# Kernel tuning notes

Measured on AMD Instinct MI355X. Metric: run time of the kernel, lower is better.

## Reference

```python
import jax, jax.numpy as jnp
import numpy as np

HEAD = 32  # HEAD_SIZE
B, T, C = 8, 1024, 768
LAYER_ID, N_LAYER = 2, 12


def wkv7(r, w, k, v, a, b):
    # RWKV7 linear recurrence (matches the custom CUDA 'attn' kernel math):
    #   S = S * exp(-exp(w)) + (S @ a) b^T + v k^T ;  y = S @ r
    Bb, Tt, Cc = r.shape
    H, N = Cc // HEAD, HEAD
    rs = lambda z: jnp.moveaxis(z.reshape(Bb, Tt, H, N), 1, 0)  # [T,B,H,N]
    rT, kT, vT, aT, bT = rs(r), rs(k), rs(v), rs(a), rs(b)
    wT = rs(jnp.exp(-jnp.exp(w)))  # decay in (0,1)
    def step(S, inp):
        rt, wt, kt, vt, at, bt = inp  # each [B,H,N]
        sa = jnp.einsum('bhij,bhj->bhi', S, at)
        S = S * wt[:, :, None, :] + sa[..., None] * bt[:, :, None, :] + vt[..., None] * kt[:, :, None, :]
        return S, jnp.einsum('bhij,bhj->bhi', S, rt)
    S0 = jnp.zeros((Bb, H, N, N), r.dtype)
    _, y = jax.lax.scan(step, S0, (rT, wT, kT, vT, aT, bT))
    return jnp.moveaxis(y, 0, 1).reshape(Bb, Tt, Cc)


def setup_inputs() -> dict:
    key = jax.random.key(0)
    ks = iter(jax.random.split(key, 64))
    def rn(shape, s=0.02):
        return (jax.random.normal(next(ks), shape, jnp.float32) * s)
    def un(shape, lim):
        return jax.random.uniform(next(ks), shape, jnp.float32, -lim, lim)
    H, N = C // HEAD, HEAD
    r10 = 1.0 - LAYER_ID / N_LAYER          # ratio_1_to_almost0
    r01 = LAYER_ID / (N_LAYER - 1)          # ratio_0_to_1
    ddd = (np.arange(C, dtype=np.float64) / C).reshape(1, 1, C)
    f32 = lambda z: jnp.asarray(z, jnp.float32)
    time_maa_x = f32(1.0 - ddd ** (0.6 * r10 ** 0.9))
    time_maa_rg = f32(1.0 - ddd ** (0.2 * r10))
    time_maa_wa = f32(1.0 - ddd ** (0.9 * r10))
    time_maa_k = f32(1.0 - (ddd ** (0.9 * r10) + 0.4 * r01))
    time_maa_v = f32(1.0 - (ddd ** (0.4 * r10) + 0.6 * r01))
    ds = -7.0 + 5.0 * (np.arange(C, dtype=np.float64) / (C - 1)) ** (0.85 + r01 ** 0.5)
    time_decay = f32(ds.reshape(1, 1, C) + 0.5)
    inp = {
        'x': jax.random.normal(next(ks), (B, T, C), jnp.float32),
        'v1': jax.random.normal(next(ks), (B, T, C), jnp.float32),
        'time_maa_x': time_maa_x, 'time_maa_rg': time_maa_rg, 'time_maa_wa': time_maa_wa,
        'time_maa_k': time_maa_k, 'time_maa_v': time_maa_v,
        'time_decay': time_decay,
        'time_faaaa': rn((1, 1, H, N), 0.05),
        'time_aaaaa': rn((1, 1, C), 0.05),
        'time_maa_w1': rn((C, 28 * 4)), 'time_maa_w2': rn((4, 28, C), 0.05),
        'time_decay_w1': rn((C, 64)), 'time_decay_w2': rn((64, C), 0.05),
        'time_aaa_w1': rn((C, 24)), 'time_aaa_w2': rn((24, C), 0.05),
        'time_kkk_w1': rn((C, 24)), 'time_kkk_w2': rn((24, C), 0.05),
        'gate_w1': rn((C, 120)), 'gate_w2': rn((120, C), 0.05),
        'ma_w1': rn((C, 24)), 'ma_w2': rn((24, C), 0.05), 'time_misc_a': rn((1, 1, C), 0.05),
        'mk_w1': rn((C, 24)), 'mk_w2': rn((24, C), 0.05), 'time_misc_k': rn((1, 1, C), 0.05),
        'mv_w1': rn((C, 24)), 'mv_w2': rn((24, C), 0.05), 'time_misc_v': 1.0 + rn((1, 1, C), 0.05),
        'Wr': un((C, C), 0.5 / C ** 0.5), 'Wk': un((C, C), 0.05 / C ** 0.5),
        'Wv': un((C, C), 0.5 / C ** 0.5), 'Wo': rn((C, C), 0.02),
        'ln_w': jnp.ones((C,), jnp.float32), 'ln_b': jnp.zeros((C,), jnp.float32),
    }
    return inp


def reference(x, v1, time_maa_x, time_maa_rg, time_maa_wa, time_maa_k, time_maa_v,
              time_decay, time_faaaa, time_aaaaa, time_maa_w1, time_maa_w2,
              time_decay_w1, time_decay_w2, time_aaa_w1, time_aaa_w2,
              time_kkk_w1, time_kkk_w2, gate_w1, gate_w2, ma_w1, ma_w2, time_misc_a,
              mk_w1, mk_w2, time_misc_k, mv_w1, mv_w2, time_misc_v,
              Wr, Wk, Wv, Wo, ln_w, ln_b):
    Bb, Tt, Cc = x.shape
    H, N = Cc // HEAD, HEAD
    # token shift: xx[t] = x[t-1] - x[t], with x[-1] = 0
    xsh = jnp.concatenate([jnp.zeros_like(x[:, :1]), x[:, :-1]], axis=1)
    xx = xsh - x
    xxx = x + xx * time_maa_x
    tm = jnp.tanh(xxx @ time_maa_w1).reshape(Bb, Tt, 4, -1)      # [B,T,4,28]
    mix = jnp.einsum('btfd,fdc->fbtc', tm, time_maa_w2)          # [4,B,T,C]
    xrg = x + xx * (time_maa_rg + mix[0])
    xwa = x + xx * (time_maa_wa + mix[1])
    xk = x + xx * (time_maa_k + mix[2])
    xv = x + xx * (time_maa_v + mix[3])
    r = xrg @ Wr
    w = -jax.nn.softplus(-(time_decay + jnp.tanh(xwa @ time_decay_w1) @ time_decay_w2)) - 0.5
    k = xk @ Wk
    v = xv @ Wv
    v = v + (v1 - v) * jax.nn.sigmoid(time_misc_v + xv @ mv_w1 @ mv_w2)
    g = jax.nn.sigmoid(xrg @ gate_w1) @ gate_w2
    kk = k + jnp.tanh(xk @ time_kkk_w1) @ time_kkk_w2
    kk4 = kk.reshape(Bb, Tt, H, N)
    nrm = jnp.maximum(jnp.sqrt(jnp.sum(kk4 * kk4, axis=-1, keepdims=True)), 1e-12)
    kk = (kk4 / nrm).reshape(Bb, Tt, Cc)
    a = jax.nn.sigmoid(time_aaaaa + xwa @ time_aaa_w1 @ time_aaa_w2)
    ma = jax.nn.sigmoid(time_misc_a + xwa @ ma_w1 @ ma_w2)
    k = k * ma + k * a * (1.0 - ma)
    mk = jax.nn.sigmoid(time_misc_k + xk @ mk_w1 @ mk_w2)
    k = k * jnp.exp(jnp.minimum(w * mk, 0.0))
    y = wkv7(r, w, k, v, -kk, kk * a)
    # GroupNorm(n_head groups) over each token, eps=6.4e-5
    yg = y.reshape(Bb, Tt, H, N)
    mu = jnp.mean(yg, axis=-1, keepdims=True)
    var = jnp.var(yg, axis=-1, keepdims=True)
    yn = (yg - mu) * jax.lax.rsqrt(var + 6.4e-05)
    yn = yn * ln_w.reshape(H, N) + ln_b.reshape(H, N)
    # per-head bonus term
    bonus = (jnp.sum(r.reshape(Bb, Tt, H, N) * k.reshape(Bb, Tt, H, N) * time_faaaa,
                     axis=-1, keepdims=True) * v.reshape(Bb, Tt, H, N))
    y = yn.reshape(Bb, Tt, Cc) + bonus.reshape(Bb, Tt, Cc)
    out = (y * g) @ Wo
    return (out, v1)
```

## Files before the change

### kernel.cpp

```cpp
#include <hip/hip_runtime.h>
#include <hip/hip_bf16.h>
#include <math.h>

#define Bdim 8
#define Tdim 1024
#define Cdim 768
#define Hdim 24
#define Ndim 32
#define BTdim (Bdim*Tdim)
#define CH6 16

typedef __attribute__((ext_vector_type(8))) short bf16x8;
typedef __attribute__((ext_vector_type(4))) float f32x4;
typedef __hip_bfloat16 bf16;

__device__ __forceinline__ float sigm(float x){ return 1.f/(1.f+expf(-x)); }
__device__ __forceinline__ float softplusf(float x){ return fmaxf(x,0.f) + log1pf(expf(-fabsf(x))); }
__device__ __forceinline__ float bf2f(bf16 v){ return __bfloat162float(v); }
__device__ __forceinline__ float us2f(unsigned short s){ return __builtin_bit_cast(float, (unsigned)s<<16); }

template<int CTRL>
__device__ __forceinline__ float dpp_add(float x){
  int xi = __builtin_bit_cast(int, x);
  int yi = __builtin_amdgcn_mov_dpp(xi, CTRL, 0xF, 0xF, true);
  return x + __builtin_bit_cast(float, yi);
}
__device__ __forceinline__ float red32(float x){
  x = dpp_add<0xB1>(x);
  x = dpp_add<0x4E>(x);
  x = dpp_add<0x141>(x);
  x = dpp_add<0x140>(x);
  x += __shfl_xor(x, 16);
  return x;
}
__device__ __forceinline__ float red16(float x){
  x = dpp_add<0xB1>(x);
  x = dpp_add<0x4E>(x);
  x = dpp_add<0x141>(x);
  x = dpp_add<0x140>(x);
  return x;
}
__device__ __forceinline__ void cvt8(uint4 u, float* d){
  d[0]=__builtin_bit_cast(float, u.x<<16); d[1]=__builtin_bit_cast(float, u.x&0xFFFF0000u);
  d[2]=__builtin_bit_cast(float, u.y<<16); d[3]=__builtin_bit_cast(float, u.y&0xFFFF0000u);
  d[4]=__builtin_bit_cast(float, u.z<<16); d[5]=__builtin_bit_cast(float, u.z&0xFFFF0000u);
  d[6]=__builtin_bit_cast(float, u.w<<16); d[7]=__builtin_bit_cast(float, u.w&0xFFFF0000u);
}

#define GLDS16(gp, lp) __builtin_amdgcn_global_load_lds((const __attribute__((address_space(1))) void*)(gp), (__attribute__((address_space(3))) void*)(lp), 16, 0, 0)

__global__ void k1_shift(const float* __restrict__ x, const float* __restrict__ maa_x,
                         float* __restrict__ xx, bf16* __restrict__ xxx) {
  int idx = blockIdx.x*256 + threadIdx.x;
  if (idx >= BTdim*Cdim) return;
  int c = idx % Cdim; int row = idx / Cdim; int t = row % Tdim;
  float xv = x[idx];
  float xp = (t==0) ? 0.f : x[idx - Cdim];
  float d = xp - xv;
  xx[idx] = d;
  xxx[idx] = __float2bfloat16(xv + d*maa_x[c]);
}

__global__ __launch_bounds__(256) void kconvW(const float* __restrict__ W0, const float* __restrict__ W1,
    const float* __restrict__ W2, const float* __restrict__ W3,
    bf16* __restrict__ T0, bf16* __restrict__ T1, bf16* __restrict__ T2, bf16* __restrict__ T3) {
  const float* Wsrc[4] = {W0,W1,W2,W3};
  bf16* Tdst[4] = {T0,T1,T2,T3};
  const float* W = Wsrc[blockIdx.z];
  bf16* T = Tdst[blockIdx.z];
  __shared__ float tile[32][33];
  int bx = blockIdx.x*32, by = blockIdx.y*32;
  int tx = threadIdx.x & 31, ty = threadIdx.x >> 5;
  #pragma unroll
  for (int q=0;q<32;q+=8) tile[ty+q][tx] = W[(size_t)(by+ty+q)*Cdim + bx+tx];
  __syncthreads();
  #pragma unroll
  for (int q=0;q<32;q+=8) T[(size_t)(bx+ty+q)*Cdim + by+tx] = __float2bfloat16(tile[tx][ty+q]);
}

__global__ __launch_bounds__(256) void kprep(const float* __restrict__ dw1, const float* __restrict__ aaa_w1,
    const float* __restrict__ ma_w1, const float* __restrict__ kkk_w1, const float* __restrict__ mk_w1,
    const float* __restrict__ mv_w1, const float* __restrict__ gate_w1, const float* __restrict__ maa_w1,
    const float* __restrict__ dw2, const float* __restrict__ aaa_w2, const float* __restrict__ ma_w2,
    const float* __restrict__ kkk_w2, const float* __restrict__ mk_w2, const float* __restrict__ mv_w2,
    const float* __restrict__ gate_w2,
    bf16* __restrict__ PWwa, bf16* __restrict__ PWk, bf16* __restrict__ PWv,
    bf16* __restrict__ PWrg, bf16* __restrict__ PWmaa,
    bf16* __restrict__ W2wa, bf16* __restrict__ W2k, bf16* __restrict__ W2v, bf16* __restrict__ W2g){
  int idx = blockIdx.x*256 + threadIdx.x;
  if (idx < 491520) {
    int buf = idx / 98304, rem = idx - buf*98304;
    int n = rem / 768, kk = rem - n*768;
    float val = 0.f;
    bf16* dst;
    switch(buf){
      case 0: dst=PWwa; if(n<64) val=dw1[(size_t)kk*64+n]; else if(n<88) val=aaa_w1[(size_t)kk*24+(n-64)]; else if(n<112) val=ma_w1[(size_t)kk*24+(n-88)]; break;
      case 1: dst=PWk;  if(n<24) val=kkk_w1[(size_t)kk*24+n]; else if(n<48) val=mk_w1[(size_t)kk*24+(n-24)]; break;
      case 2: dst=PWv;  if(n<24) val=mv_w1[(size_t)kk*24+n]; break;
      case 3: dst=PWrg; if(n<120) val=gate_w1[(size_t)kk*120+n]; break;
      default: dst=PWmaa; if(n<112) val=maa_w1[(size_t)kk*112+n]; break;
    }
    dst[rem] = __float2bfloat16(val);
    return;
  }
  int i = idx - 491520;
  if (i < 294912){
    int n=i>>7, q=i&127, seg=n/768, c=n-seg*768;
    float val=0.f;
    if (seg==0){ if(q<64) val=dw2[(size_t)q*768+c]; }
    else if (seg==1){ if(q>=64&&q<88) val=aaa_w2[(size_t)(q-64)*768+c]; }
    else { if(q>=88&&q<112) val=ma_w2[(size_t)(q-88)*768+c]; }
    W2wa[i]=__float2bfloat16(val); return;
  }
  i -= 294912;
  if (i < 98304){
    int n=i>>6, q=i&63, seg=n/768, c=n-seg*768;
    float val=0.f;
    if (seg==0){ if(q<24) val=kkk_w2[(size_t)q*768+c]; }
    else { if(q>=24&&q<48) val=mk_w2[(size_t)(q-24)*768+c]; }
    W2k[i]=__float2bfloat16(val); return;
  }
  i -= 98304;
  if (i < 24576){
    int c=i>>5, q=i&31;
    float val = (q<24) ? mv_w2[(size_t)q*768+c] : 0.f;
    W2v[i]=__float2bfloat16(val); return;
  }
  i -= 24576;
  if (i < 98304){
    int c=i>>7, q=i&127;
    float val = (q<120) ? gate_w2[(size_t)q*768+c] : 0.f;
    W2g[i]=__float2bfloat16(val);
  }
}

template<typename OutT>
__global__ __launch_bounds__(256) void gemm_mfma(const bf16* __restrict__ A,
    const bf16* __restrict__ Bt, OutT* __restrict__ C, int M, int N, int K) {
  __shared__ unsigned short As[128*32];
  __shared__ unsigned short Bs[128*32];
  const int bm = blockIdx.y*128, bn = blockIdx.x*128;
  const int tid = threadIdx.x, lane = tid&63, w = tid>>6;
  const int wr = w>>1, wc = w&1;
  const int lr = lane&15, kg = lane>>4;
  f32x4 zero = {0.f,0.f,0.f,0.f};
  f32x4 acc[4][4];
  #pragma unroll
  for (int m=0;m<4;m++)
    #pragma unroll
    for (int n=0;n<4;n++) acc[m][n]=zero;
  const size_t rowA = (size_t)(bm + w*32 + (lane>>2))*K + (lane&3)*8;
  const size_t rowB = (size_t)(bn + w*32 + (lane>>2))*K + (lane&3)*8;
  unsigned short* lA = As + w*32*32;
  unsigned short* lB = Bs + w*32*32;
  for (int k0=0; k0<K; k0+=32){
    GLDS16(A + rowA + k0,                 lA);
    GLDS16(A + rowA + k0 + (size_t)16*K,  lA + 512);
    GLDS16(Bt + rowB + k0,                lB);
    GLDS16(Bt + rowB + k0 + (size_t)16*K, lB + 512);
    __syncthreads();
    bf16x8 af[4], bfr[4];
    #pragma unroll
    for (int m=0;m<4;m++) af[m]  = *(const bf16x8*)(void*)(As + (wr*64+m*16+lr)*32 + kg*8);
    #pragma unroll
    for (int n=0;n<4;n++) bfr[n] = *(const bf16x8*)(void*)(Bs + (wc*64+n*16+lr)*32 + kg*8);
    #pragma unroll
    for (int m=0;m<4;m++)
      #pragma unroll
      for (int n=0;n<4;n++)
        acc[m][n] = __builtin_amdgcn_mfma_f32_16x16x32_bf16(af[m], bfr[n], acc[m][n], 0,0,0);
    __syncthreads();
  }
  #pragma unroll
  for (int m=0;m<4;m++)
    #pragma unroll
    for (int n=0;n<4;n++){
      size_t r0 = (size_t)(bm + wr*64 + m*16 + kg*4);
      int cc = bn + wc*64 + n*16 + lr;
      #pragma unroll
      for (int q=0;q<4;q++){
        float val = acc[m][n][q];
        if constexpr (sizeof(OutT)==2) C[(r0+q)*N + cc] = __float2bfloat16(val);
        else                           C[(r0+q)*N + cc] = val;
      }
    }
}

__global__ __launch_bounds__(256) void gemm_tm(const bf16* __restrict__ A,
    const bf16* __restrict__ Bt, float* __restrict__ C, int K) {
  __shared__ unsigned short As[128*32];
  __shared__ unsigned short Bs[128*32];
  const int bm = blockIdx.y*128;
  const int tid = threadIdx.x, lane = tid&63, w = tid>>6;
  const int wr = w>>1, wc = w&1;
  const int lr = lane&15, kg = lane>>4;
  f32x4 zero = {0.f,0.f,0.f,0.f};
  f32x4 acc[4][4];
  #pragma unroll
  for (int m=0;m<4;m++)
    #pragma unroll
    for (int n=0;n<4;n++) acc[m][n]=zero;
  const size_t rowA = (size_t)(bm + w*32 + (lane>>2))*K + (lane&3)*8;
  const size_t rowB = (size_t)(w*32 + (lane>>2))*K + (lane&3)*8;
  unsigned short* lA = As + w*32*32;
  unsigned short* lB = Bs + w*32*32;
  for (int k0=0; k0<K; k0+=32){
    GLDS16(A + rowA + k0,                 lA);
    GLDS16(A + rowA + k0 + (size_t)16*K,  lA + 512);
    GLDS16(Bt + rowB + k0,                lB);
    GLDS16(Bt + rowB + k0 + (size_t)16*K, lB + 512);
    __syncthreads();
    bf16x8 af[4], bfr[4];
    #pragma unroll
    for (int m=0;m<4;m++) af[m]  = *(const bf16x8*)(void*)(As + (wr*64+m*16+lr)*32 + kg*8);
    #pragma unroll
    for (int n=0;n<4;n++) bfr[n] = *(const bf16x8*)(void*)(Bs + (wc*64+n*16+lr)*32 + kg*8);
    #pragma unroll
    for (int m=0;m<4;m++)
      #pragma unroll
      for (int n=0;n<4;n++)
        acc[m][n] = __builtin_amdgcn_mfma_f32_16x16x32_bf16(af[m], bfr[n], acc[m][n], 0,0,0);
    __syncthreads();
  }
  #pragma unroll
  for (int m=0;m<4;m++)
    #pragma unroll
    for (int n=0;n<4;n++){
      size_t r0 = (size_t)(bm + wr*64 + m*16 + kg*4);
      int cc = wc*64 + n*16 + lr;
      if (cc < 112){
        #pragma unroll
        for (int q=0;q<4;q++)
          C[(r0+q)*112 + cc] = tanhf(acc[m][n][q]);
      }
    }
}

struct S1P {
  const bf16* A[4];
  const bf16* Bt[4];
  bf16* C[4];
  int Ntrue[4];
  int Nalloc[4];
  int act[4];
};
__global__ __launch_bounds__(256) void gemm_s1(S1P p, int K) {
  const int z = blockIdx.z;
  const bf16* __restrict__ A  = p.A[z];
  const bf16* __restrict__ Bt = p.Bt[z];
  bf16* __restrict__ C = p.C[z];
  const int Ntrue = p.Ntrue[z], Nalloc = p.Nalloc[z], act = p.act[z];
  __shared__ unsigned short As[128*32];
  __shared__ unsigned short Bs[128*32];
  const int bm = blockIdx.y*128;
  const int tid = threadIdx.x, lane = tid&63, w = tid>>6;
  const int wr = w>>1, wc = w&1;
  const int lr = lane&15, kg = lane>>4;
  f32x4 zero = {0.f,0.f,0.f,0.f};
  f32x4 acc[4][4];
  #pragma unroll
  for (int m=0;m<4;m++)
    #pragma unroll
    for (int n=0;n<4;n++) acc[m][n]=zero;
  const size_t rowA = (size_t)(bm + w*32 + (lane>>2))*K + (lane&3)*8;
  const size_t rowB = (size_t)(w*32 + (lane>>2))*K + (lane&3)*8;
  unsigned short* lA = As + w*32*32;
  unsigned short* lB = Bs + w*32*32;
  for (int k0=0; k0<K; k0+=32){
    GLDS16(A + rowA + k0,                 lA);
    GLDS16(A + rowA + k0 + (size_t)16*K,  lA + 512);
    GLDS16(Bt + rowB + k0,                lB);
    GLDS16(Bt + rowB + k0 + (size_t)16*K, lB + 512);
    __syncthreads();
    bf16x8 af[4], bfr[4];
    #pragma unroll
    for (int m=0;m<4;m++) af[m]  = *(const bf16x8*)(void*)(As + (wr*64+m*16+lr)*32 + kg*8);
    #pragma unroll
    for (int n=0;n<4;n++) bfr[n] = *(const bf16x8*)(void*)(Bs + (wc*64+n*16+lr)*32 + kg*8);
    #pragma unroll
    for (int m=0;m<4;m++)
      #pragma unroll
      for (int n=0;n<4;n++)
        acc[m][n] = __builtin_amdgcn_mfma_f32_16x16x32_bf16(af[m], bfr[n], acc[m][n], 0,0,0);
    __syncthreads();
  }
  #pragma unroll
  for (int m=0;m<4;m++)
    #pragma unroll
    for (int n=0;n<4;n++){
      size_t r0 = (size_t)(bm + wr*64 + m*16 + kg*4);
      int cc = wc*64 + n*16 + lr;
      if (cc < Nalloc){
        #pragma unroll
        for (int q=0;q<4;q++){
          float val = acc[m][n][q];
          if      (act==1){ if (cc<64) val = tanhf(val); }
          else if (act==2){ if (cc<24) val = tanhf(val); }
          else if (act==3){ val = sigm(val); }
          if (cc >= Ntrue) val = 0.f;
          C[(r0+q)*Nalloc + cc] = __float2bfloat16(val);
        }
      }
    }
}

struct Z4 {
  const bf16* A[4];
  const bf16* Bt[4];
  bf16* C[4];
  int N[4];
  int K[4];
};
__global__ __launch_bounds__(256) void gemm_z(Z4 p) {
  const int z = blockIdx.z;
  const int N = p.N[z], K = p.K[z];
  const int bn = blockIdx.x*128;
  if (bn >= N) return;
  const bf16* __restrict__ A  = p.A[z];
  const bf16* __restrict__ Bt = p.Bt[z];
  bf16* __restrict__ C = p.C[z];
  __shared__ unsigned short As[128*32];
  __shared__ unsigned short Bs[128*32];
  const int bm = blockIdx.y*128;
  const int tid = threadIdx.x, lane = tid&63, w = tid>>6;
  const int wr = w>>1, wc = w&1;
  const int lr = lane&15, kg = lane>>4;
  f32x4 zero = {0.f,0.f,0.f,0.f};
  f32x4 acc[4][4];
  #pragma unroll
  for (int m=0;m<4;m++)
    #pragma unroll
    for (int n=0;n<4;n++) acc[m][n]=zero;
  const size_t rowA = (size_t)(bm + w*32 + (lane>>2))*K + (lane&3)*8;
  const size_t rowB = (size_t)(bn + w*32 + (lane>>2))*K + (lane&3)*8;
  unsigned short* lA = As + w*32*32;
  unsigned short* lB = Bs + w*32*32;
  for (int k0=0; k0<K; k0+=32){
    GLDS16(A + rowA + k0,                 lA);
    GLDS16(A + rowA + k0 + (size_t)16*K,  lA + 512);
    GLDS16(Bt + rowB + k0,                lB);
    GLDS16(Bt + rowB + k0 + (size_t)16*K, lB + 512);
    __syncthreads();
    bf16x8 af[4], bfr[4];
    #pragma unroll
    for (int m=0;m<4;m++) af[m]  = *(const bf16x8*)(void*)(As + (wr*64+m*16+lr)*32 + kg*8);
    #pragma unroll
    for (int n=0;n<4;n++) bfr[n] = *(const bf16x8*)(void*)(Bs + (wc*64+n*16+lr)*32 + kg*8);
    #pragma unroll
    for (int m=0;m<4;m++)
      #pragma unroll
      for (int n=0;n<4;n++)
        acc[m][n] = __builtin_amdgcn_mfma_f32_16x16x32_bf16(af[m], bfr[n], acc[m][n], 0,0,0);
    __syncthreads();
  }
  #pragma unroll
  for (int m=0;m<4;m++)
    #pragma unroll
    for (int n=0;n<4;n++){
      size_t r0 = (size_t)(bm + wr*64 + m*16 + kg*4);
      int cc = bn + wc*64 + n*16 + lr;
      #pragma unroll
      for (int q=0;q<4;q++)
        C[(r0+q)*N + cc] = __float2bfloat16(acc[m][n][q]);
    }
}

__global__ __launch_bounds__(256) void k2_mix(const float* __restrict__ x, const float* __restrict__ xx,
    const float* __restrict__ tm, const float* __restrict__ w2,
    const float* __restrict__ mrg, const float* __restrict__ mwa,
    const float* __restrict__ mk_, const float* __restrict__ mv_,
    bf16* __restrict__ xrg, bf16* __restrict__ xwa, bf16* __restrict__ xk, bf16* __restrict__ xv) {
  const int row0 = blockIdx.x*8, tid = threadIdx.x;
  __shared__ float stm[8][112];
  for (int idx=tid; idx<8*112; idx+=256){
    int rr=idx/112, q=idx-rr*112;
    stm[rr][q]=tm[(size_t)(row0+rr)*112+q];
  }
  __syncthreads();
  for (int c=tid;c<Cdim;c+=256){
    float x8[8], d8[8];
    #pragma unroll
    for (int rr=0;rr<8;rr++){
      size_t i=(size_t)(row0+rr)*Cdim+c;
      x8[rr]=x[i]; d8[rr]=xx[i];
    }
    float mrgc=mrg[c], mwac=mwa[c], mkc=mk_[c], mvc=mv_[c];
    float m0[8]={},m1[8]={},m2[8]={},m3[8]={};
    #pragma unroll 4
    for (int d=0; d<28; d++){
      float w0=w2[(size_t)(d)*Cdim + c];
      float w1=w2[(size_t)(28+d)*Cdim + c];
      float w2v=w2[(size_t)(56+d)*Cdim + c];
      float w3=w2[(size_t)(84+d)*Cdim + c];
      #pragma unroll
      for (int rr=0;rr<8;rr++){
        m0[rr]+=stm[rr][d]*w0; m1[rr]+=stm[rr][28+d]*w1;
        m2[rr]+=stm[rr][56+d]*w2v; m3[rr]+=stm[rr][84+d]*w3;
      }
    }
    #pragma unroll
    for (int rr=0;rr<8;rr++){
      size_t i=(size_t)(row0+rr)*Cdim+c;
      xrg[i]=__float2bfloat16(x8[rr] + d8[rr]*(mrgc+m0[rr]));
      xwa[i]=__float2bfloat16(x8[rr] + d8[rr]*(mwac+m1[rr]));
      xk[i] =__float2bfloat16(x8[rr] + d8[rr]*(mkc+m2[rr]));
      xv[i] =__float2bfloat16(x8[rr] + d8[rr]*(mvc+m3[rr]));
    }
  }
}

__global__ __launch_bounds__(256) void k5_fuse(
    const bf16* __restrict__ zwa, const bf16* __restrict__ zk, const bf16* __restrict__ zv,
    const float* __restrict__ td, const float* __restrict__ aaaaa,
    const float* __restrict__ misc_a, const float* __restrict__ misc_k, const float* __restrict__ misc_v,
    const float* __restrict__ v1,
    float* __restrict__ kbuf, float* __restrict__ vbuf, float* __restrict__ wexp,
    bf16* __restrict__ kb_bf, bf16* __restrict__ vb_bf,
    bf16* __restrict__ akv, bf16* __restrict__ bkv) {
  const int row = blockIdx.x, tid = threadIdx.x;
  float kraw[3], v0[3], v1v[3];
  #pragma unroll
  for (int it=0;it<3;it++){
    size_t i=(size_t)row*Cdim + tid + it*256;
    kraw[it]=kbuf[i]; v0[it]=vbuf[i]; v1v[it]=v1[i];
  }
  __syncthreads();
  #pragma unroll
  for (int it=0;it<3;it++){
    const int c = tid + it*256;
    const size_t i=(size_t)row*Cdim+c;
    float zd = bf2f(zwa[(size_t)row*2304 + c]);
    float za = bf2f(zwa[(size_t)row*2304 + 768 + c]);
    float zma= bf2f(zwa[(size_t)row*2304 + 1536 + c]);
    float zkk= bf2f(zk[(size_t)row*1536 + c]);
    float zmk= bf2f(zk[(size_t)row*1536 + 768 + c]);
    float zmv= bf2f(zv[i]);
    float w = -softplusf(-(td[c]+zd)) - 0.5f;
    wexp[i] = expf(-expf(w));
    float a  = sigm(aaaaa[c]+za);
    float ma = sigm(misc_a[c]+zma);
    float mk = sigm(misc_k[c]+zmk);
    float mv = sigm(misc_v[c]+zmv);
    vb_bf[i] = __float2bfloat16(v0[it] + (v1v[it]-v0[it])*mv);
    float kf = kraw[it]*(ma + a*(1.f-ma))*expf(fminf(w*mk,0.f));
    kb_bf[i] = __float2bfloat16(kf);
    float kk = kraw[it] + zkk;
    float ss = red32(kk*kk);
    float kkn = kk * (1.f/fmaxf(sqrtf(ss),1e-12f));
    akv[i] = __float2bfloat16(-kkn);
    bkv[i] = __float2bfloat16(kkn*a);
  }
}

__global__ __launch_bounds__(64) void k6_wkv(const unsigned short* __restrict__ r, const float* __restrict__ wd,
    const unsigned short* __restrict__ k, const unsigned short* __restrict__ v,
    const unsigned short* __restrict__ a, const unsigned short* __restrict__ b2, float* __restrict__ y) {
  const int lane = threadIdx.x;
  const int bid = blockIdx.x;
  const int head = bid % (Bdim*Hdim);
  const int rq   = bid / (Bdim*Hdim);
  const int bb = head / Hdim, hh = head - bb*Hdim;
  const int rl = lane >> 4;
  const int i0 = rq*4 + rl;
  const int jh = lane & 15;
  const int col = jh*2;
  __shared__ __align__(16) float swd[2][CH6][Ndim];
  __shared__ __align__(16) unsigned short sbf[2][4][CH6][Ndim];
  __shared__ __align__(16) unsigned short sv2[2][CH6][Ndim];
  const unsigned short* gb16[4] = {r, k, a, b2};
  const size_t gbase = (size_t)bb*Tdim*Cdim + (size_t)hh*Ndim;
  float S0=0.f, S1=0.f;

  auto STAGE = [&](int c, int buf){
    const size_t tb = (size_t)c*CH6;
    GLDS16(wd + gbase + (tb +   (lane>>3))*Cdim + (lane&7)*4, &swd[buf][0][0]);
    GLDS16(wd + gbase + (tb + 8+(lane>>3))*Cdim + (lane&7)*4, &swd[buf][8][0]);
    #pragma unroll
    for (int arr=0; arr<4; arr++)
      GLDS16(gb16[arr] + gbase + (tb + (lane>>2))*Cdim + (lane&3)*8, &sbf[buf][arr][0][0]);
    GLDS16(v + gbase + (tb + (lane>>2))*Cdim + (lane&3)*8, &sv2[buf][0][0]);
  };

  unsigned nr, nk, na, nb; float2 nw; unsigned short nv;
  auto LOADT = [&](int buf, int t){
    nr = *(const unsigned*)&sbf[buf][0][t][col];
    nk = *(const unsigned*)&sbf[buf][1][t][col];
    na = *(const unsigned*)&sbf[buf][2][t][col];
    nb = *(const unsigned*)&sbf[buf][3][t][col];
    nw = *(const float2*)&swd[buf][t][col];
    nv = sv2[buf][t][i0];
  };

  STAGE(0, 0);
  asm volatile("s_waitcnt vmcnt(0)" ::: "memory");
  LOADT(0, 0);
  int buf = 0;
  const int NCH = Tdim/CH6;
  for (int c=0; c<NCH; ++c){
    if (c+1 < NCH) STAGE(c+1, buf^1);
    const size_t yb = gbase + (size_t)c*CH6*Cdim;
    #pragma unroll
    for (int t=0; t<CH6; t++){
      unsigned cr=nr, ck=nk, ca=na, cb=nb;
      float2 cw=nw;
      unsigned short cv=nv;
      if (t < CH6-1) LOADT(buf, t+1);
      float a0 = __builtin_bit_cast(float, ca<<16);
      float a1 = __builtin_bit_cast(float, ca&0xFFFF0000u);
      float sa = S0*a0 + S1*a1;
      sa = red16(sa);
      float k0 = __builtin_bit_cast(float, ck<<16);
      float k1 = __builtin_bit_cast(float, ck&0xFFFF0000u);
      float b0 = __builtin_bit_cast(float, cb<<16);
      float b1 = __builtin_bit_cast(float, cb&0xFFFF0000u);
      float r0 = __builtin_bit_cast(float, cr<<16);
      float r1 = __builtin_bit_cast(float, cr&0xFFFF0000u);
      const float vl = us2f(cv);
      S0 = S0*cw.x + (sa*b0 + vl*k0);
      S1 = S1*cw.y + (sa*b1 + vl*k1);
      float yv = S0*r0 + S1*r1;
      yv = red16(yv);
      if (jh == 0) y[yb + (size_t)t*Cdim + i0] = yv;
      if (t == CH6-1 && c+1 < NCH){
        asm volatile("s_waitcnt vmcnt(0)" ::: "memory");
        LOADT(buf^1, 0);
      }
    }
    buf ^= 1;
  }
}

__global__ __launch_bounds__(256) void k7_post(const float* __restrict__ y,
    const bf16* __restrict__ r, const bf16* __restrict__ kf, const bf16* __restrict__ v,
    const bf16* __restrict__ g, const float* __restrict__ faaaa,
    const float* __restrict__ lnw, const float* __restrict__ lnb,
    bf16* __restrict__ ygate) {
  const int row = blockIdx.x, tid = threadIdx.x;
  #pragma unroll
  for (int it=0; it<3; it++){
    const int c = tid + it*256;
    const size_t i = (size_t)row*Cdim + c;
    float yv = y[i];
    float bon = bf2f(r[i])*bf2f(kf[i])*faaaa[c];
    float s  = red32(yv);
    float ss = red32(yv*yv);
    float bn = red32(bon);
    float mu = s*(1.f/Ndim);
    float var = ss*(1.f/Ndim) - mu*mu;
    float rs = rsqrtf(var + 6.4e-5f);
    float yn = (yv-mu)*rs*lnw[c]+lnb[c];
    ygate[i]=__float2bfloat16((yn + bn*bf2f(v[i]))*bf2f(g[i]));
  }
}

__global__ void k9_copy(const float4* __restrict__ src, float4* __restrict__ dst){
  int idx = blockIdx.x*256 + threadIdx.x;
  if (idx < BTdim*Cdim/4) dst[idx]=src[idx];
}

extern "C" void kernel_launch(void* const* d_in, const int* in_sizes, int n_in,
                              void* d_out, int out_size, void* d_ws, size_t ws_size,
                              hipStream_t stream) {
  const float* x      = (const float*)d_in[0];
  const float* v1     = (const float*)d_in[1];
  const float* maa_x  = (const float*)d_in[2];
  const float* maa_rg = (const float*)d_in[3];
  const float* maa_wa = (const float*)d_in[4];
  const float* maa_k  = (const float*)d_in[5];
  const float* maa_v  = (const float*)d_in[6];
  const float* time_decay = (const float*)d_in[7];
  const float* faaaa  = (const float*)d_in[8];
  const float* aaaaa  = (const float*)d_in[9];
  const float* maa_w1 = (const float*)d_in[10];
  const float* maa_w2 = (const float*)d_in[11];
  const float* dw1    = (const float*)d_in[12];
  const float* dw2    = (const float*)d_in[13];
  const float* aaa_w1 = (const float*)d_in[14];
  const float* aaa_w2 = (const float*)d_in[15];
  const float* kkk_w1 = (const float*)d_in[16];
  const float* kkk_w2 = (const float*)d_in[17];
  const float* gate_w1= (const float*)d_in[18];
  const float* gate_w2= (const float*)d_in[19];
  const float* ma_w1  = (const float*)d_in[20];
  const float* ma_w2  = (const float*)d_in[21];
  const float* misc_a = (const float*)d_in[22];
  const float* mk_w1  = (const float*)d_in[23];
  const float* mk_w2  = (const float*)d_in[24];
  const float* misc_k = (const float*)d_in[25];
  const float* mv_w1  = (const float*)d_in[26];
  const float* mv_w2  = (const float*)d_in[27];
  const float* misc_v = (const float*)d_in[28];
  const float* Wr     = (const float*)d_in[29];
  const float* Wk     = (const float*)d_in[30];
  const float* Wv     = (const float*)d_in[31];
  const float* Wo     = (const float*)d_in[32];
  const float* lnw    = (const float*)d_in[33];
  const float* lnb    = (const float*)d_in[34];
  float* out = (float*)d_out;

  float* ws = (float*)d_ws;
  const size_t BTC = (size_t)BTdim*Cdim;
  const size_t HB  = BTC/2;
  float* xx   = ws;                float* wexp = ws;
  float* kb   = ws + 2*HB;         bf16* kb_bf = (bf16*)kb;
  float* vb   = ws + 4*HB;         bf16* vb_bf = (bf16*)vb;
  bf16* xrg_bf = (bf16*)(ws + 6*HB);
  bf16* xwa_bf = xrg_bf + BTC;
  bf16* zwa_bf = (bf16*)(ws + 6*HB);
  bf16* xk_bf  = (bf16*)(ws + 9*HB);
  bf16* xv_bf  = xk_bf + BTC;
  bf16* zk_bf  = (bf16*)(ws + 9*HB);
  bf16* xxx_bf = (bf16*)(ws + 11*HB);
  bf16* zv_bf  = (bf16*)(ws + 11*HB);
  float* tm    = ws + 12*HB;
  bf16* zg_bf  = (bf16*)(ws + 12*HB);
  bf16* hwa_bf = (bf16*)(ws + 13*HB);
  bf16* hk_bf  = hwa_bf + (size_t)BTdim*128;
  bf16* hv_bf  = hk_bf  + (size_t)BTdim*64;
  bf16* hrg_bf = hv_bf  + (size_t)BTdim*32;
  bf16* akv_bf = (bf16*)(ws + 13*HB);
  bf16* bkv_bf = (bf16*)(ws + 14*HB);
  bf16* yg_bf  = (bf16*)(ws + 14*HB);
  float* ybuf  = ws + 15*HB;
  bf16* rb_bf  = (bf16*)(ws + 17*HB);
  bf16* Wbase  = (bf16*)(ws + 18*HB);
  bf16* WtR = Wbase;
  bf16* WtK = WtR + 589824;
  bf16* WtV = WtK + 589824;
  bf16* WtO = WtV + 589824;
  bf16* PWwa = WtO + 589824;
  bf16* PWk  = PWwa + 98304;
  bf16* PWv  = PWk  + 98304;
  bf16* PWrg = PWv  + 98304;
  bf16* PWmaa= PWrg + 98304;
  bf16* W2wa = PWmaa + 98304;
  bf16* W2k  = W2wa + 294912;
  bf16* W2v  = W2k  + 98304;
  bf16* W2g  = W2v  + 24576;

  dim3 blk(256);
  kconvW<<<dim3(24,24,4), blk, 0, stream>>>(Wr,Wk,Wv,Wo, WtR,WtK,WtV,WtO);
  kprep<<<dim3(3936), blk, 0, stream>>>(dw1,aaa_w1,ma_w1,kkk_w1,mk_w1,mv_w1,gate_w1,maa_w1,
                                        dw2,aaa_w2,ma_w2,kkk_w2,mk_w2,mv_w2,gate_w2,
                                        PWwa,PWk,PWv,PWrg,PWmaa, W2wa,W2k,W2v,W2g);
  k1_shift<<<dim3((BTdim*Cdim+255)/256), blk, 0, stream>>>(x, maa_x, xx, xxx_bf);
  gemm_tm<<<dim3(1,64), blk, 0, stream>>>(xxx_bf, PWmaa, tm, Cdim);
  k2_mix<<<dim3(BTdim/8), blk, 0, stream>>>(x, xx, tm, maa_w2, maa_rg, maa_wa, maa_k, maa_v,
                                            xrg_bf, xwa_bf, xk_bf, xv_bf);
  {
    S1P p{};
    p.A[0]=xwa_bf; p.Bt[0]=PWwa; p.C[0]=hwa_bf; p.Ntrue[0]=112; p.Nalloc[0]=128; p.act[0]=1;
    p.A[1]=xk_bf;  p.Bt[1]=PWk;  p.C[1]=hk_bf;  p.Ntrue[1]=48;  p.Nalloc[1]=64;  p.act[1]=2;
    p.A[2]=xv_bf;  p.Bt[2]=PWv;  p.C[2]=hv_bf;  p.Ntrue[2]=24;  p.Nalloc[2]=32;  p.act[2]=0;
    p.A[3]=xrg_bf; p.Bt[3]=PWrg; p.C[3]=hrg_bf; p.Ntrue[3]=120; p.Nalloc[3]=128; p.act[3]=3;
    gemm_s1<<<dim3(1,64,4), blk, 0, stream>>>(p, Cdim);
  }
  gemm_mfma<bf16> <<<dim3(6,64), blk, 0, stream>>>(xrg_bf, WtR, rb_bf, BTdim, Cdim, Cdim);
  gemm_mfma<float><<<dim3(6,64), blk, 0, stream>>>(xk_bf,  WtK, kb,    BTdim, Cdim, Cdim);
  gemm_mfma<float><<<dim3(6,64), blk, 0, stream>>>(xv_bf,  WtV, vb,    BTdim, Cdim, Cdim);
  {
    Z4 p{};
    p.A[0]=hwa_bf; p.Bt[0]=W2wa; p.C[0]=zwa_bf; p.N[0]=2304; p.K[0]=128;
    p.A[1]=hk_bf;  p.Bt[1]=W2k;  p.C[1]=zk_bf;  p.N[1]=1536; p.K[1]=64;
    p.A[2]=hv_bf;  p.Bt[2]=W2v;  p.C[2]=zv_bf;  p.N[2]=768;  p.K[2]=32;
    p.A[3]=hrg_bf; p.Bt[3]=W2g;  p.C[3]=zg_bf;  p.N[3]=768;  p.K[3]=128;
    gemm_z<<<dim3(18,64,4), blk, 0, stream>>>(p);
  }
  k5_fuse<<<dim3(BTdim), blk, 0, stream>>>(zwa_bf, zk_bf, zv_bf,
      time_decay, aaaaa, misc_a, misc_k, misc_v, v1,
      kb, vb, wexp, kb_bf, vb_bf, akv_bf, bkv_bf);
  k6_wkv<<<dim3(Bdim*Hdim*8), dim3(64), 0, stream>>>((const unsigned short*)rb_bf, wexp,
      (const unsigned short*)kb_bf, (const unsigned short*)vb_bf,
      (const unsigned short*)akv_bf, (const unsigned short*)bkv_bf, ybuf);
  k7_post<<<dim3(BTdim), blk, 0, stream>>>(ybuf, rb_bf, kb_bf, vb_bf, zg_bf, faaaa, lnw, lnb, yg_bf);
  gemm_mfma<float><<<dim3(6,64), blk, 0, stream>>>(yg_bf, WtO, out, BTdim, Cdim, Cdim);
  k9_copy<<<dim3(BTdim*Cdim/4/256), blk, 0, stream>>>((const float4*)v1, (float4*)(out + BTC));
}
```

Baseline: 538.2 us.

## Batch R/K/V GEMMs into one launch, fold v1 copy, deepen WKV prefetch

The three separate 768x768 projection GEMMs are merged into one grid-z-indexed launch, with a per-slice flag choosing bf16 or fp32 output. This cuts launch count and lets the three GEMMs share the GPU at the same time. The standalone v1 copy kernel is folded into k7_post, so each row block also copies its slice of v1. The WKV recurrence now prefetches LDS operands two timesteps ahead with double-buffered register sets, moving the chunk-boundary wait earlier, at the cost of more registers.

```diff
diff --git a/kernel.cpp b/kernel.cpp
--- a/kernel.cpp
+++ b/kernel.cpp
@@ -39,12 +39,6 @@
   x = dpp_add<0x141>(x);
   x = dpp_add<0x140>(x);
   return x;
-}
-__device__ __forceinline__ void cvt8(uint4 u, float* d){
-  d[0]=__builtin_bit_cast(float, u.x<<16); d[1]=__builtin_bit_cast(float, u.x&0xFFFF0000u);
-  d[2]=__builtin_bit_cast(float, u.y<<16); d[3]=__builtin_bit_cast(float, u.y&0xFFFF0000u);
-  d[4]=__builtin_bit_cast(float, u.z<<16); d[5]=__builtin_bit_cast(float, u.z&0xFFFF0000u);
-  d[6]=__builtin_bit_cast(float, u.w<<16); d[7]=__builtin_bit_cast(float, u.w&0xFFFF0000u);
 }
 
 #define GLDS16(gp, lp) __builtin_amdgcn_global_load_lds((const __attribute__((address_space(1))) void*)(gp), (__attribute__((address_space(3))) void*)(lp), 16, 0, 0)
@@ -134,9 +128,8 @@
   }
 }
 
-template<typename OutT>
 __global__ __launch_bounds__(256) void gemm_mfma(const bf16* __restrict__ A,
-    const bf16* __restrict__ Bt, OutT* __restrict__ C, int M, int N, int K) {
+    const bf16* __restrict__ Bt, float* __restrict__ C, int M, int N, int K) {
   __shared__ unsigned short As[128*32];
   __shared__ unsigned short Bs[128*32];
   const int bm = blockIdx.y*128, bn = blockIdx.x*128;
@@ -178,12 +171,82 @@
       size_t r0 = (size_t)(bm + wr*64 + m*16 + kg*4);
       int cc = bn + wc*64 + n*16 + lr;
       #pragma unroll
-      for (int q=0;q<4;q++){
-        float val = acc[m][n][q];
-        if constexpr (sizeof(OutT)==2) C[(r0+q)*N + cc] = __float2bfloat16(val);
-        else                           C[(r0+q)*N + cc] = val;
+      for (int q=0;q<4;q++)
+        C[(r0+q)*N + cc] = acc[m][n][q];
+    }
+}
+
+struct G3 {
+  const bf16* A[3];
+  const bf16* Bt[3];
+  float* Cf[3];
+  bf16* Ch[3];
+  int isbf[3];
+};
+__global__ __launch_bounds__(256) void gemm_big3(G3 p, int N, int K) {
+  const int z = blockIdx.z;
+  const bf16* __restrict__ A  = p.A[z];
+  const bf16* __restrict__ Bt = p.Bt[z];
+  const int isbf = p.isbf[z];
+  __shared__ unsigned short As[128*32];
+  __shared__ unsigned short Bs[128*32];
+  const int bm = blockIdx.y*128, bn = blockIdx.x*128;
+  const int tid = threadIdx.x, lane = tid&63, w = tid>>6;
+  const int wr = w>>1, wc = w&1;
+  const int lr = lane&15, kg = lane>>4;
+  f32x4 zero = {0.f,0.f,0.f,0.f};
+  f32x4 acc[4][4];
+  #pragma unroll
+  for (int m=0;m<4;m++)
+    #pragma unroll
+    for (int n=0;n<4;n++) acc[m][n]=zero;
+  const size_t rowA = (size_t)(bm + w*32 + (lane>>2))*K + (lane&3)*8;
+  const size_t rowB = (size_t)(bn + w*32 + (lane>>2))*K + (lane&3)*8;
+  unsigned short* lA = As + w*32*32;
+  unsigned short* lB = Bs + w*32*32;
+  for (int k0=0; k0<K; k0+=32){
+    GLDS16(A + rowA + k0,                 lA);
+    GLDS16(A + rowA + k0 + (size_t)16*K,  lA + 512);
+    GLDS16(Bt + rowB + k0,                lB);
+    GLDS16(Bt + rowB + k0 + (size_t)16*K, lB + 512);
+    __syncthreads();
+    bf16x8 af[4], bfr[4];
+    #pragma unroll
+    for (int m=0;m<4;m++) af[m]  = *(const bf16x8*)(void*)(As + (wr*64+m*16+lr)*32 + kg*8);
+    #pragma unroll
+    for (int n=0;n<4;n++) bfr[n] = *(const bf16x8*)(void*)(Bs + (wc*64+n*16+lr)*32 + kg*8);
+    #pragma unroll
+    for (int m=0;m<4;m++)
+      #pragma unroll
+      for (int n=0;n<4;n++)
+        acc[m][n] = __builtin_amdgcn_mfma_f32_16x16x32_bf16(af[m], bfr[n], acc[m][n], 0,0,0);
+    __syncthreads();
+  }
+  if (isbf){
+    bf16* __restrict__ C = p.Ch[z];
+    #pragma unroll
+    for (int m=0;m<4;m++)
+      #pragma unroll
+      for (int n=0;n<4;n++){
+        size_t r0 = (size_t)(bm + wr*64 + m*16 + kg*4);
+        int cc = bn + wc*64 + n*16 + lr;
+        #pragma unroll
+        for (int q=0;q<4;q++)
+          C[(r0+q)*N + cc] = __float2bfloat16(acc[m][n][q]);
       }
-    }
+  } else {
+    float* __restrict__ C = p.Cf[z];
+    #pragma unroll
+    for (int m=0;m<4;m++)
+      #pragma unroll
+      for (int n=0;n<4;n++){
+        size_t r0 = (size_t)(bm + wr*64 + m*16 + kg*4);
+        int cc = bn + wc*64 + n*16 + lr;
+        #pragma unroll
+        for (int q=0;q<4;q++)
+          C[(r0+q)*N + cc] = acc[m][n][q];
+      }
+  }
 }
 
 __global__ __launch_bounds__(256) void gemm_tm(const bf16* __restrict__ A,
@@ -452,6 +515,7 @@
   }
 }
 
+struct TReg { unsigned r,k,a,b; float2 w; unsigned short v; };
 __global__ __launch_bounds__(64) void k6_wkv(const unsigned short* __restrict__ r, const float* __restrict__ wd,
     const unsigned short* __restrict__ k, const unsigned short* __restrict__ v,
     const unsigned short* __restrict__ a, const unsigned short* __restrict__ b2, float* __restrict__ y) {
@@ -460,8 +524,7 @@
   const int head = bid % (Bdim*Hdim);
   const int rq   = bid / (Bdim*Hdim);
   const int bb = head / Hdim, hh = head - bb*Hdim;
-  const int rl = lane >> 4;
-  const int i0 = rq*4 + rl;
+  const int i0 = rq*4 + (lane >> 4);
   const int jh = lane & 15;
   const int col = jh*2;
   __shared__ __align__(16) float swd[2][CH6][Ndim];
@@ -481,19 +544,20 @@
     GLDS16(v + gbase + (tb + (lane>>2))*Cdim + (lane&3)*8, &sv2[buf][0][0]);
   };
 
-  unsigned nr, nk, na, nb; float2 nw; unsigned short nv;
-  auto LOADT = [&](int buf, int t){
-    nr = *(const unsigned*)&sbf[buf][0][t][col];
-    nk = *(const unsigned*)&sbf[buf][1][t][col];
-    na = *(const unsigned*)&sbf[buf][2][t][col];
-    nb = *(const unsigned*)&sbf[buf][3][t][col];
-    nw = *(const float2*)&swd[buf][t][col];
-    nv = sv2[buf][t][i0];
+  auto LOADT = [&](TReg& d, int buf, int t){
+    d.r = *(const unsigned*)&sbf[buf][0][t][col];
+    d.k = *(const unsigned*)&sbf[buf][1][t][col];
+    d.a = *(const unsigned*)&sbf[buf][2][t][col];
+    d.b = *(const unsigned*)&sbf[buf][3][t][col];
+    d.w = *(const float2*)&swd[buf][t][col];
+    d.v = sv2[buf][t][i0];
   };
 
   STAGE(0, 0);
   asm volatile("s_waitcnt vmcnt(0)" ::: "memory");
-  LOADT(0, 0);
+  TReg pA, pB;
+  LOADT(pA, 0, 0);
+  LOADT(pB, 0, 1);
   int buf = 0;
   const int NCH = Tdim/CH6;
   for (int c=0; c<NCH; ++c){
@@ -501,10 +565,17 @@
     const size_t yb = gbase + (size_t)c*CH6*Cdim;
     #pragma unroll
     for (int t=0; t<CH6; t++){
-      unsigned cr=nr, ck=nk, ca=na, cb=nb;
-      float2 cw=nw;
-      unsigned short cv=nv;
-      if (t < CH6-1) LOADT(buf, t+1);
+      TReg& cur = (t&1) ? pB : pA;
+      const unsigned cr=cur.r, ck=cur.k, ca=cur.a, cb=cur.b;
+      const float2 cw=cur.w;
+      const unsigned short cv=cur.v;
+      const int tt = t+2;
+      if (tt < CH6) {
+        LOADT(cur, buf, tt);
+      } else if (c+1 < NCH) {
+        if (tt == CH6) asm volatile("s_waitcnt vmcnt(0)" ::: "memory");
+        LOADT(cur, buf^1, tt-CH6);
+      }
       float a0 = __builtin_bit_cast(float, ca<<16);
       float a1 = __builtin_bit_cast(float, ca&0xFFFF0000u);
       float sa = S0*a0 + S1*a1;
@@ -521,10 +592,6 @@
       float yv = S0*r0 + S1*r1;
       yv = red16(yv);
       if (jh == 0) y[yb + (size_t)t*Cdim + i0] = yv;
-      if (t == CH6-1 && c+1 < NCH){
-        asm volatile("s_waitcnt vmcnt(0)" ::: "memory");
-        LOADT(buf^1, 0);
-      }
     }
     buf ^= 1;
   }
@@ -534,8 +601,10 @@
     const bf16* __restrict__ r, const bf16* __restrict__ kf, const bf16* __restrict__ v,
     const bf16* __restrict__ g, const float* __restrict__ faaaa,
     const float* __restrict__ lnw, const float* __restrict__ lnb,
-    bf16* __restrict__ ygate) {
+    bf16* __restrict__ ygate,
+    const float4* __restrict__ v1c, float4* __restrict__ outc) {
   const int row = blockIdx.x, tid = threadIdx.x;
+  if (tid < 192) outc[(size_t)row*192 + tid] = v1c[(size_t)row*192 + tid];
   #pragma unroll
   for (int it=0; it<3; it++){
     const int c = tid + it*256;
@@ -551,11 +620,6 @@
     float yn = (yv-mu)*rs*lnw[c]+lnb[c];
     ygate[i]=__float2bfloat16((yn + bn*bf2f(v[i]))*bf2f(g[i]));
   }
-}
-
-__global__ void k9_copy(const float4* __restrict__ src, float4* __restrict__ dst){
-  int idx = blockIdx.x*256 + threadIdx.x;
-  if (idx < BTdim*Cdim/4) dst[idx]=src[idx];
 }
 
 extern "C" void kernel_launch(void* const* d_in, const int* in_sizes, int n_in,
@@ -655,9 +719,13 @@
     p.A[3]=xrg_bf; p.Bt[3]=PWrg; p.C[3]=hrg_bf; p.Ntrue[3]=120; p.Nalloc[3]=128; p.act[3]=3;
     gemm_s1<<<dim3(1,64,4), blk, 0, stream>>>(p, Cdim);
   }
-  gemm_mfma<bf16> <<<dim3(6,64), blk, 0, stream>>>(xrg_bf, WtR, rb_bf, BTdim, Cdim, Cdim);
-  gemm_mfma<float><<<dim3(6,64), blk, 0, stream>>>(xk_bf,  WtK, kb,    BTdim, Cdim, Cdim);
-  gemm_mfma<float><<<dim3(6,64), blk, 0, stream>>>(xv_bf,  WtV, vb,    BTdim, Cdim, Cdim);
+  {
+    G3 p{};
+    p.A[0]=xrg_bf; p.Bt[0]=WtR; p.Ch[0]=rb_bf; p.Cf[0]=nullptr; p.isbf[0]=1;
+    p.A[1]=xk_bf;  p.Bt[1]=WtK; p.Cf[1]=kb;    p.Ch[1]=nullptr; p.isbf[1]=0;
+    p.A[2]=xv_bf;  p.Bt[2]=WtV; p.Cf[2]=vb;    p.Ch[2]=nullptr; p.isbf[2]=0;
+    gemm_big3<<<dim3(6,64,3), blk, 0, stream>>>(p, Cdim, Cdim);
+  }
   {
     Z4 p{};
     p.A[0]=hwa_bf; p.Bt[0]=W2wa; p.C[0]=zwa_bf; p.N[0]=2304; p.K[0]=128;
@@ -672,7 +740,7 @@
   k6_wkv<<<dim3(Bdim*Hdim*8), dim3(64), 0, stream>>>((const unsigned short*)rb_bf, wexp,
       (const unsigned short*)kb_bf, (const unsigned short*)vb_bf,
       (const unsigned short*)akv_bf, (const unsigned short*)bkv_bf, ybuf);
-  k7_post<<<dim3(BTdim), blk, 0, stream>>>(ybuf, rb_bf, kb_bf, vb_bf, zg_bf, faaaa, lnw, lnb, yg_bf);
-  gemm_mfma<float><<<dim3(6,64), blk, 0, stream>>>(yg_bf, WtO, out, BTdim, Cdim, Cdim);
-  k9_copy<<<dim3(BTdim*Cdim/4/256), blk, 0, stream>>>((const float4*)v1, (float4*)(out + BTC));
-}
+  k7_post<<<dim3(BTdim), blk, 0, stream>>>(ybuf, rb_bf, kb_bf, vb_bf, zg_bf, faaaa, lnw, lnb, yg_bf,
+                                           (const float4*)v1, (float4*)(out + BTC));
+  gemm_mfma<<<dim3(6,64), blk, 0, stream>>>(yg_bf, WtO, out, BTdim, Cdim, Cdim);
+}
```

Measured after the change: 527.1 us. 2.1% less time.
